# Optimization experiments

Measured on AMD Instinct MI355X. Metric: run time of the kernel, lower is better.

The kernel has to match this reference:

```python
import jax, jax.numpy as jnp
import numpy as np

N_EMBED = 1024
N_HEADS = 16
HEAD_DIM = N_EMBED // N_HEADS


def setup_inputs() -> dict:
    key = jax.random.key(0)
    ks = jax.random.split(key, 5)
    x = jax.random.normal(ks[0], (4, 2048, N_EMBED), dtype=jnp.float32)
    # Linear params (torch nn.Linear: y = x @ W.T + b); store W as [in, out]
    s = 1.0 / np.sqrt(N_EMBED)
    W_attn = jax.random.uniform(ks[1], (N_EMBED, 3 * N_EMBED), minval=-s, maxval=s, dtype=jnp.float32)
    b_attn = jax.random.uniform(ks[2], (3 * N_EMBED,), minval=-s, maxval=s, dtype=jnp.float32)
    W_proj = jax.random.uniform(ks[3], (N_EMBED, N_EMBED), minval=-s, maxval=s, dtype=jnp.float32)
    b_proj = jax.random.uniform(ks[4], (N_EMBED,), minval=-s, maxval=s, dtype=jnp.float32)
    return {"x": x, "W_attn": W_attn, "b_attn": b_attn, "W_proj": W_proj, "b_proj": b_proj}


def reference(x, W_attn, b_attn, W_proj, b_proj):
    B, L, D = x.shape
    H, Hd = N_HEADS, HEAD_DIM
    qkv = x @ W_attn + b_attn  # [B, L, 3D]
    q, k, v = jnp.split(qkv, 3, axis=-1)
    q = q.reshape(B, L, H, Hd).transpose(0, 2, 1, 3)  # [B, H, L, Hd]
    k = k.reshape(B, L, H, Hd).transpose(0, 2, 1, 3)
    v = v.reshape(B, L, H, Hd).transpose(0, 2, 1, 3)
    scores = jnp.einsum('bhqd,bhkd->bhqk', q, k) / jnp.sqrt(jnp.float32(Hd))
    causal = jnp.tril(jnp.ones((L, L), dtype=bool))
    scores = jnp.where(causal[None, None], scores, -jnp.inf)
    probs = jax.nn.softmax(scores.astype(jnp.float32), axis=-1).astype(x.dtype)
    o = jnp.einsum('bhqk,bhkd->bhqd', probs, v)  # [B, H, L, Hd]
    o = o.transpose(0, 2, 1, 3).reshape(B, L, D)
    return o @ W_proj + b_proj
```

## Files before the change

### kernel.cpp

```cpp
#include <hip/hip_runtime.h>


typedef __attribute__((ext_vector_type(8))) short short8;
typedef __attribute__((ext_vector_type(4))) short s16x4;
typedef __attribute__((ext_vector_type(4))) float f32x4;

#define DEVI __device__ __forceinline__

constexpr int NE = 1024, NH = 16, NB = 4, L = 2048;
constexpr int M = NB * L;
constexpr int KD = 1024;

DEVI unsigned f2bf(float f) {
    union { float f; unsigned u; } v; v.f = f;
    unsigned u = v.u;
    u += 0x7fffu + ((u >> 16) & 1u);
    return u >> 16;
}
DEVI unsigned pack_bf2(float lo, float hi) {
    union { float f; unsigned u; } a, b; a.f = lo; b.f = hi;
    return ((a.u + 0x8000u) >> 16) | ((b.u + 0x8000u) & 0xffff0000u);
}

typedef const __attribute__((address_space(1))) void* gas_t;
typedef __attribute__((address_space(3))) void* las_t;
DEVI void gl_lds16(const void* g, void* l) {
    __builtin_amdgcn_global_load_lds((gas_t)g, (las_t)l, 16, 0, 0);
}

__global__ void k_f32_to_bf16(const float* __restrict__ in,
                              unsigned short* __restrict__ out, int n8) {
    int i = blockIdx.x * blockDim.x + threadIdx.x;
    if (i >= n8) return;
    const float4* p = (const float4*)in + (size_t)i * 2;
    float4 a = p[0], b = p[1];
    short8 r;
    r[0] = f2bf(a.x); r[1] = f2bf(a.y); r[2] = f2bf(a.z); r[3] = f2bf(a.w);
    r[4] = f2bf(b.x); r[5] = f2bf(b.y); r[6] = f2bf(b.z); r[7] = f2bf(b.w);
    ((short8*)out)[i] = r;
}

__global__ void k_transpose_bf16(const float* __restrict__ in,
                                 unsigned short* __restrict__ out, int R, int C) {
    __shared__ float t[32][33];
    int x = blockIdx.x * 32 + threadIdx.x;
    int y0 = blockIdx.y * 32;
#pragma unroll
    for (int i = 0; i < 4; i++)
        t[threadIdx.y + 8 * i][threadIdx.x] = in[(size_t)(y0 + threadIdx.y + 8 * i) * C + x];
    __syncthreads();
    int xo = y0 + threadIdx.x;
    int yo = blockIdx.x * 32 + threadIdx.y;
#pragma unroll
    for (int i = 0; i < 4; i++)
        out[(size_t)(yo + 8 * i) * R + xo] = f2bf(t[threadIdx.x][threadIdx.y + 8 * i]);
}

template <int MODE>
__global__ __launch_bounds__(256, 4)
void k_gemm(const unsigned short* __restrict__ A,
            const unsigned short* __restrict__ Bt,
            const float* __restrict__ bias,
            unsigned short* __restrict__ Qb,
            unsigned short* __restrict__ Kb,
            unsigned short* __restrict__ Vt,
            float* __restrict__ out) {
    __shared__ alignas(16) short As[128 * 64];
    __shared__ alignas(16) short Bs[128 * 64];
    const int tid = threadIdx.x;
    const int lane = tid & 63, wid = tid >> 6;
    const int quad = lane >> 4, l16 = lane & 15;
    const int wm = (wid >> 1) * 64, wn = (wid & 1) * 64;
    const int m0 = blockIdx.y * 128;
    const int n0 = blockIdx.x * 128;

    const int srow = lane >> 3;
    const int gseg = (lane & 7) ^ srow;

    f32x4 acc[4][4] = {};

    for (int kk = 0; kk < KD; kk += 64) {
        __syncthreads();
#pragma unroll
        for (int c = 0; c < 4; c++) {
            const int rbase = c * 32 + wid * 8;
            gl_lds16(&A[(size_t)(m0 + rbase + srow) * KD + kk + gseg * 8], &As[rbase * 64]);
            gl_lds16(&Bt[(size_t)(n0 + rbase + srow) * KD + kk + gseg * 8], &Bs[rbase * 64]);
        }
        __syncthreads();
#pragma unroll
        for (int kc = 0; kc < 2; kc++) {
            short8 af[4], bf[4];
#pragma unroll
            for (int t = 0; t < 4; t++) {
                const int Ra = wm + t * 16 + l16;
                af[t] = *(const short8*)&As[Ra * 64 + (((kc * 4 + quad) ^ (Ra & 7)) * 8)];
                const int Rb = wn + t * 16 + l16;
                bf[t] = *(const short8*)&Bs[Rb * 64 + (((kc * 4 + quad) ^ (Rb & 7)) * 8)];
            }
#pragma unroll
            for (int mt = 0; mt < 4; mt++)
#pragma unroll
                for (int nt = 0; nt < 4; nt++)
                    acc[mt][nt] = __builtin_amdgcn_mfma_f32_16x16x32_bf16(
                        af[mt], bf[nt], acc[mt][nt], 0, 0, 0);
        }
    }

#pragma unroll
    for (int nt = 0; nt < 4; nt++) {
        const int n = n0 + wn + nt * 16 + l16;
        const float bv = bias[n];
        if (MODE == 0) {
            const int sel = n >> 10;
            const int h = (n & 1023) >> 6;
            const int d = n & 63;
#pragma unroll
            for (int mt = 0; mt < 4; mt++)
#pragma unroll
                for (int r = 0; r < 4; r++) {
                    const int m = m0 + wm + mt * 16 + quad * 4 + r;
                    const int b = m >> 11, l = m & 2047;
                    const int bh = b * NH + h;
                    const float v = acc[mt][nt][r] + bv;
                    if (sel == 0)      Qb[(size_t)(bh * L + l) * 64 + d] = f2bf(v * 0.125f);
                    else if (sel == 1) Kb[(size_t)(bh * L + l) * 64 + d] = f2bf(v);
                    else               Vt[(size_t)(bh * 64 + d) * L + l] = f2bf(v);
                }
        } else {
#pragma unroll
            for (int mt = 0; mt < 4; mt++)
#pragma unroll
                for (int r = 0; r < 4; r++) {
                    const int m = m0 + wm + mt * 16 + quad * 4 + r;
                    out[(size_t)m * NE + n] = acc[mt][nt][r] + bv;
                }
        }
    }
}

__global__ __launch_bounds__(256, 4)
void k_attn(const unsigned short* __restrict__ Q,
            const unsigned short* __restrict__ Kb,
            const unsigned short* __restrict__ Vt,
            unsigned short* __restrict__ O) {
    __shared__ alignas(16) short smem[16384];
    short* Ks = smem;
    short* Vs = smem + 8192;
    short* Os = smem;

    const int tid = threadIdx.x;
    const int lane = tid & 63, wid = tid >> 6;
    const int quad = lane >> 4, l16 = lane & 15;
    const int bh = blockIdx.x;
    const int qb = 15 - (int)blockIdx.y;
    const int q0 = qb * 128 + wid * 32;
    const size_t base = (size_t)bh * L * 64;
    const int b = bh >> 4, h = bh & 15;

    const int srowK = lane >> 3;
    const int gsegK = (lane & 7) ^ srowK;
    const int vrow_off = (lane >> 4);
    const int vseg = lane & 15;

    short8 qf[2][2];
#pragma unroll
    for (int mt = 0; mt < 2; mt++)
#pragma unroll
        for (int dc = 0; dc < 2; dc++)
            qf[mt][dc] = *(const short8*)&Q[base + (size_t)(q0 + mt * 16 + l16) * 64 + dc * 32 + quad * 8];

    f32x4 o[2][4] = {};
    float lrow[2] = {0.f, 0.f};

    for (int kt = 0; kt <= qb; kt++) {
        __syncthreads();
#pragma unroll
        for (int c = 0; c < 4; c++) {
            const int rbase = c * 32 + wid * 8;
            gl_lds16(&Kb[base + (size_t)(kt * 128 + rbase + srowK) * 64 + gsegK * 8],
                     &Ks[rbase * 64]);
        }
#pragma unroll
        for (int c = 0; c < 4; c++) {
            const int rbase = c * 16 + wid * 4;
            const int row = rbase + vrow_off;
            const int gs = vseg ^ (row & 15);
            gl_lds16(&Vt[base + (size_t)row * L + kt * 128 + gs * 8], &Vs[rbase * 128]);
        }
        __syncthreads();

        const bool diag = (kt == qb);
        const int chunks = diag ? (wid + 1) : 4;

        for (int kc = 0; kc < chunks; kc++) {
            short8 kf[2][2];
#pragma unroll
            for (int j0 = 0; j0 < 2; j0++)
#pragma unroll
                for (int dc = 0; dc < 2; dc++) {
                    const int R = kc * 32 + j0 * 16 + l16;
                    kf[j0][dc] = *(const short8*)&Ks[R * 64 + (((dc * 4 + quad) ^ (R & 7)) * 8)];
                }
            f32x4 st[2][2];
#pragma unroll
            for (int mt = 0; mt < 2; mt++)
#pragma unroll
                for (int j0 = 0; j0 < 2; j0++) {
                    f32x4 z = {};
                    z = __builtin_amdgcn_mfma_f32_16x16x32_bf16(kf[j0][0], qf[mt][0], z, 0, 0, 0);
                    z = __builtin_amdgcn_mfma_f32_16x16x32_bf16(kf[j0][1], qf[mt][1], z, 0, 0, 0);
                    st[mt][j0] = z;
                }
            const bool dm = diag && (kc == wid);
            short8 pb[2];
#pragma unroll
            for (int mt = 0; mt < 2; mt++) {
                float pe[8];
                float sum = 0.f;
#pragma unroll
                for (int j0 = 0; j0 < 2; j0++)
#pragma unroll
                    for (int r = 0; r < 4; r++) {
                        float p = __expf(st[mt][j0][r]);
                        if (dm) {
                            const int krel = j0 * 16 + quad * 4 + r;
                            const int qrel = mt * 16 + l16;
                            if (krel > qrel) p = 0.f;
                        }
                        sum += p;
                        pe[j0 * 4 + r] = p;
                    }
                lrow[mt] += sum;
#pragma unroll
                for (int w = 0; w < 4; w++) {
                    unsigned pk = pack_bf2(pe[2 * w], pe[2 * w + 1]);
                    pb[mt][2 * w] = (short)(pk & 0xffff);
                    pb[mt][2 * w + 1] = (short)(pk >> 16);
                }
            }
#pragma unroll
            for (int dt = 0; dt < 4; dt++) {
                const int R2 = dt * 16 + l16;
                const int s16a = kc * 4 + (quad >> 1);
                const int off = (quad & 1) * 4;
                s16x4 lo = *(const s16x4*)&Vs[R2 * 128 + ((s16a ^ l16) * 8) + off];
                s16x4 hi = *(const s16x4*)&Vs[R2 * 128 + (((s16a + 2) ^ l16) * 8) + off];
                short8 vf = __builtin_shufflevector(lo, hi, 0, 1, 2, 3, 4, 5, 6, 7);
#pragma unroll
                for (int mt = 0; mt < 2; mt++)
                    o[mt][dt] = __builtin_amdgcn_mfma_f32_16x16x32_bf16(
                        vf, pb[mt], o[mt][dt], 0, 0, 0);
            }
        }
    }

    float inv[2];
#pragma unroll
    for (int mt = 0; mt < 2; mt++) {
        float rs = lrow[mt];
        rs += __shfl_xor(rs, 16);
        rs += __shfl_xor(rs, 32);
        inv[mt] = 1.0f / rs;
    }

    __syncthreads();
#pragma unroll
    for (int mt = 0; mt < 2; mt++) {
        const int ql = wid * 32 + mt * 16 + l16;
#pragma unroll
        for (int dt = 0; dt < 4; dt++) {
            unsigned w0 = f2bf(o[mt][dt][0] * inv[mt]) | (f2bf(o[mt][dt][1] * inv[mt]) << 16);
            unsigned w1 = f2bf(o[mt][dt][2] * inv[mt]) | (f2bf(o[mt][dt][3] * inv[mt]) << 16);
            *(uint2*)&Os[ql * 72 + dt * 16 + quad * 4] = make_uint2(w0, w1);
        }
    }
    __syncthreads();
#pragma unroll
    for (int i = 0; i < 4; i++) {
        const int id = i * 256 + tid;
        const int row = id >> 3, seg = id & 7;
        short8 v = *(const short8*)&Os[row * 72 + seg * 8];
        const int q = qb * 128 + row;
        *(short8*)&O[(size_t)(b * L + q) * NE + h * 64 + seg * 8] = v;
    }
}

extern "C" void kernel_launch(void* const* d_in, const int* in_sizes, int n_in,
                              void* d_out, int out_size, void* d_ws, size_t ws_size,
                              hipStream_t stream) {
    const float* x  = (const float*)d_in[0];
    const float* Wa = (const float*)d_in[1];
    const float* ba = (const float*)d_in[2];
    const float* Wp = (const float*)d_in[3];
    const float* bp = (const float*)d_in[4];
    float* out = (float*)d_out;

    char* ws = (char*)d_ws;
    unsigned short* xb  = (unsigned short*)(ws);
    unsigned short* WaT = (unsigned short*)(ws + (16u << 20));
    unsigned short* WpT = (unsigned short*)(ws + (22u << 20));
    unsigned short* Qb  = (unsigned short*)(ws + (24u << 20));
    unsigned short* Kb  = (unsigned short*)(ws + (40u << 20));
    unsigned short* Vt  = (unsigned short*)(ws + (56u << 20));

    k_f32_to_bf16<<<(M * NE / 8 + 255) / 256, 256, 0, stream>>>(x, xb, M * NE / 8);
    k_transpose_bf16<<<dim3(3 * NE / 32, NE / 32), dim3(32, 8), 0, stream>>>(Wa, WaT, NE, 3 * NE);
    k_transpose_bf16<<<dim3(NE / 32, NE / 32), dim3(32, 8), 0, stream>>>(Wp, WpT, NE, NE);

    k_gemm<0><<<dim3(3 * NE / 128, M / 128), 256, 0, stream>>>(xb, WaT, ba, Qb, Kb, Vt, nullptr);

    unsigned short* Ob = xb;
    k_attn<<<dim3(NB * NH, 16), 256, 0, stream>>>(Qb, Kb, Vt, Ob);

    k_gemm<1><<<dim3(NE / 128, M / 128), 256, 0, stream>>>(Ob, WpT, bp, nullptr, nullptr, nullptr, out);
}
```

Measured before the change: 259.9 us.

## Double-buffer GEMM and attention LDS staging, enlarge attention query tile

The GEMM now splits each 64-wide K step into two 32-wide stages held in two LDS buffers. The next stage is fetched while MFMAs run on the current one. The attention kernel gives each block 256 queries (64 per wave) instead of 128 and double-buffers its K/V tiles so the next tile loads during compute. Causal masking now uses per-chunk absolute indices. The change targets global-load latency and doubles K/V reuse per load, at the cost of twice the LDS and registers in attention, which lowers occupancy (launch bounds go from 4 to 2).

```diff
diff --git a/kernel.cpp b/kernel.cpp
--- a/kernel.cpp
+++ b/kernel.cpp
@@ -65,8 +65,8 @@
             unsigned short* __restrict__ Kb,
             unsigned short* __restrict__ Vt,
             float* __restrict__ out) {
-    __shared__ alignas(16) short As[128 * 64];
-    __shared__ alignas(16) short Bs[128 * 64];
+    __shared__ alignas(16) short As[2][128 * 32];
+    __shared__ alignas(16) short Bs[2][128 * 32];
     const int tid = threadIdx.x;
     const int lane = tid & 63, wid = tid >> 6;
     const int quad = lane >> 4, l16 = lane & 15;
@@ -74,37 +74,46 @@
     const int m0 = blockIdx.y * 128;
     const int n0 = blockIdx.x * 128;
 
-    const int srow = lane >> 3;
-    const int gseg = (lane & 7) ^ srow;
+    const int srow = lane >> 2;
+    const int sseg = lane & 3;
 
     f32x4 acc[4][4] = {};
 
+    auto stage = [&](int buf, int kk) {
+#pragma unroll
+        for (int c = 0; c < 2; c++) {
+            const int rb = c * 64 + wid * 16;
+            const int row = rb + srow;
+            const int gs = sseg ^ (row & 3);
+            gl_lds16(&A[(size_t)(m0 + row) * KD + kk + gs * 8], &As[buf][rb * 32]);
+            gl_lds16(&Bt[(size_t)(n0 + row) * KD + kk + gs * 8], &Bs[buf][rb * 32]);
+        }
+    };
+    auto compute = [&](int buf) {
+        short8 af[4], bf[4];
+#pragma unroll
+        for (int t = 0; t < 4; t++) {
+            const int Ra = wm + t * 16 + l16;
+            af[t] = *(const short8*)&As[buf][Ra * 32 + ((quad ^ (Ra & 3)) * 8)];
+            const int Rb = wn + t * 16 + l16;
+            bf[t] = *(const short8*)&Bs[buf][Rb * 32 + ((quad ^ (Rb & 3)) * 8)];
+        }
+#pragma unroll
+        for (int mt = 0; mt < 4; mt++)
+#pragma unroll
+            for (int nt = 0; nt < 4; nt++)
+                acc[mt][nt] = __builtin_amdgcn_mfma_f32_16x16x32_bf16(
+                    af[mt], bf[nt], acc[mt][nt], 0, 0, 0);
+    };
+
+    stage(0, 0);
     for (int kk = 0; kk < KD; kk += 64) {
         __syncthreads();
-#pragma unroll
-        for (int c = 0; c < 4; c++) {
-            const int rbase = c * 32 + wid * 8;
-            gl_lds16(&A[(size_t)(m0 + rbase + srow) * KD + kk + gseg * 8], &As[rbase * 64]);
-            gl_lds16(&Bt[(size_t)(n0 + rbase + srow) * KD + kk + gseg * 8], &Bs[rbase * 64]);
-        }
+        if (kk + 32 < KD) stage(1, kk + 32);
+        compute(0);
         __syncthreads();
-#pragma unroll
-        for (int kc = 0; kc < 2; kc++) {
-            short8 af[4], bf[4];
-#pragma unroll
-            for (int t = 0; t < 4; t++) {
-                const int Ra = wm + t * 16 + l16;
-                af[t] = *(const short8*)&As[Ra * 64 + (((kc * 4 + quad) ^ (Ra & 7)) * 8)];
-                const int Rb = wn + t * 16 + l16;
-                bf[t] = *(const short8*)&Bs[Rb * 64 + (((kc * 4 + quad) ^ (Rb & 7)) * 8)];
-            }
-#pragma unroll
-            for (int mt = 0; mt < 4; mt++)
-#pragma unroll
-                for (int nt = 0; nt < 4; nt++)
-                    acc[mt][nt] = __builtin_amdgcn_mfma_f32_16x16x32_bf16(
-                        af[mt], bf[nt], acc[mt][nt], 0, 0, 0);
-        }
+        if (kk + 64 < KD) stage(0, kk + 64);
+        compute(1);
     }
 
 #pragma unroll
@@ -139,59 +148,65 @@
     }
 }
 
-__global__ __launch_bounds__(256, 4)
+__global__ __launch_bounds__(256, 2)
 void k_attn(const unsigned short* __restrict__ Q,
             const unsigned short* __restrict__ Kb,
             const unsigned short* __restrict__ Vt,
             unsigned short* __restrict__ O) {
-    __shared__ alignas(16) short smem[16384];
-    short* Ks = smem;
-    short* Vs = smem + 8192;
+    __shared__ alignas(16) short smem[32768];
+    short* Ksb = smem;
+    short* Vsb = smem + 16384;
     short* Os = smem;
 
     const int tid = threadIdx.x;
     const int lane = tid & 63, wid = tid >> 6;
     const int quad = lane >> 4, l16 = lane & 15;
     const int bh = blockIdx.x;
-    const int qb = 15 - (int)blockIdx.y;
-    const int q0 = qb * 128 + wid * 32;
+    const int qt = 7 - (int)blockIdx.y;
+    const int wq0 = qt * 256 + wid * 64;
     const size_t base = (size_t)bh * L * 64;
     const int b = bh >> 4, h = bh & 15;
 
-    const int srowK = lane >> 3;
-    const int gsegK = (lane & 7) ^ srowK;
-    const int vrow_off = (lane >> 4);
-    const int vseg = lane & 15;
-
-    short8 qf[2][2];
-#pragma unroll
-    for (int mt = 0; mt < 2; mt++)
+    short8 qf[4][2];
+#pragma unroll
+    for (int mt = 0; mt < 4; mt++)
 #pragma unroll
         for (int dc = 0; dc < 2; dc++)
-            qf[mt][dc] = *(const short8*)&Q[base + (size_t)(q0 + mt * 16 + l16) * 64 + dc * 32 + quad * 8];
-
-    f32x4 o[2][4] = {};
-    float lrow[2] = {0.f, 0.f};
-
-    for (int kt = 0; kt <= qb; kt++) {
+            qf[mt][dc] = *(const short8*)&Q[base + (size_t)(wq0 + mt * 16 + l16) * 64 + dc * 32 + quad * 8];
+
+    f32x4 o[4][4] = {};
+    float lrow[4] = {};
+
+    const int ntiles = 2 * qt + 2;
+
+    auto stage = [&](int buf, int kt) {
+        short* Kc = Ksb + buf * 8192;
+        short* Vc = Vsb + buf * 8192;
+#pragma unroll
+        for (int c = 0; c < 4; c++) {
+            const int rb = c * 32 + wid * 8;
+            const int row = rb + (lane >> 3);
+            const int gs = (lane & 7) ^ (row & 7);
+            gl_lds16(&Kb[base + (size_t)(kt * 128 + row) * 64 + gs * 8], &Kc[rb * 64]);
+        }
+#pragma unroll
+        for (int c = 0; c < 4; c++) {
+            const int rb = c * 16 + wid * 4;
+            const int row = rb + (lane >> 4);
+            const int gs = (lane & 15) ^ (row & 15);
+            gl_lds16(&Vt[base + (size_t)row * L + kt * 128 + gs * 8], &Vc[rb * 128]);
+        }
+    };
+
+    stage(0, 0);
+    for (int kt = 0; kt < ntiles; kt++) {
         __syncthreads();
-#pragma unroll
-        for (int c = 0; c < 4; c++) {
-            const int rbase = c * 32 + wid * 8;
-            gl_lds16(&Kb[base + (size_t)(kt * 128 + rbase + srowK) * 64 + gsegK * 8],
-                     &Ks[rbase * 64]);
-        }
-#pragma unroll
-        for (int c = 0; c < 4; c++) {
-            const int rbase = c * 16 + wid * 4;
-            const int row = rbase + vrow_off;
-            const int gs = vseg ^ (row & 15);
-            gl_lds16(&Vt[base + (size_t)row * L + kt * 128 + gs * 8], &Vs[rbase * 128]);
-        }
-        __syncthreads();
-
-        const bool diag = (kt == qb);
-        const int chunks = diag ? (wid + 1) : 4;
+        if (kt + 1 < ntiles) stage((kt + 1) & 1, kt + 1);
+        const short* Kc = Ksb + (kt & 1) * 8192;
+        const short* Vc = Vsb + (kt & 1) * 8192;
+
+        const int avail = wq0 + 64 - kt * 128;
+        const int chunks = avail <= 0 ? 0 : (avail >= 128 ? 4 : ((avail + 31) >> 5));
 
         for (int kc = 0; kc < chunks; kc++) {
             short8 kf[2][2];
@@ -200,11 +215,11 @@
 #pragma unroll
                 for (int dc = 0; dc < 2; dc++) {
                     const int R = kc * 32 + j0 * 16 + l16;
-                    kf[j0][dc] = *(const short8*)&Ks[R * 64 + (((dc * 4 + quad) ^ (R & 7)) * 8)];
-                }
-            f32x4 st[2][2];
-#pragma unroll
-            for (int mt = 0; mt < 2; mt++)
+                    kf[j0][dc] = *(const short8*)&Kc[R * 64 + (((dc * 4 + quad) ^ (R & 7)) * 8)];
+                }
+            f32x4 st[4][2];
+#pragma unroll
+            for (int mt = 0; mt < 4; mt++)
 #pragma unroll
                 for (int j0 = 0; j0 < 2; j0++) {
                     f32x4 z = {};
@@ -212,10 +227,10 @@
                     z = __builtin_amdgcn_mfma_f32_16x16x32_bf16(kf[j0][1], qf[mt][1], z, 0, 0, 0);
                     st[mt][j0] = z;
                 }
-            const bool dm = diag && (kc == wid);
-            short8 pb[2];
-#pragma unroll
-            for (int mt = 0; mt < 2; mt++) {
+            short8 pb[4];
+#pragma unroll
+            for (int mt = 0; mt < 4; mt++) {
+                const bool dm = (kt * 128 + kc * 32 + 31) > (wq0 + mt * 16);
                 float pe[8];
                 float sum = 0.f;
 #pragma unroll
@@ -224,9 +239,9 @@
                     for (int r = 0; r < 4; r++) {
                         float p = __expf(st[mt][j0][r]);
                         if (dm) {
-                            const int krel = j0 * 16 + quad * 4 + r;
-                            const int qrel = mt * 16 + l16;
-                            if (krel > qrel) p = 0.f;
+                            const int kcol = kt * 128 + kc * 32 + j0 * 16 + quad * 4 + r;
+                            const int q = wq0 + mt * 16 + l16;
+                            if (kcol > q) p = 0.f;
                         }
                         sum += p;
                         pe[j0 * 4 + r] = p;
@@ -244,20 +259,20 @@
                 const int R2 = dt * 16 + l16;
                 const int s16a = kc * 4 + (quad >> 1);
                 const int off = (quad & 1) * 4;
-                s16x4 lo = *(const s16x4*)&Vs[R2 * 128 + ((s16a ^ l16) * 8) + off];
-                s16x4 hi = *(const s16x4*)&Vs[R2 * 128 + (((s16a + 2) ^ l16) * 8) + off];
+                s16x4 lo = *(const s16x4*)&Vc[R2 * 128 + ((s16a ^ l16) * 8) + off];
+                s16x4 hi = *(const s16x4*)&Vc[R2 * 128 + (((s16a + 2) ^ l16) * 8) + off];
                 short8 vf = __builtin_shufflevector(lo, hi, 0, 1, 2, 3, 4, 5, 6, 7);
 #pragma unroll
-                for (int mt = 0; mt < 2; mt++)
+                for (int mt = 0; mt < 4; mt++)
                     o[mt][dt] = __builtin_amdgcn_mfma_f32_16x16x32_bf16(
                         vf, pb[mt], o[mt][dt], 0, 0, 0);
             }
         }
     }
 
-    float inv[2];
-#pragma unroll
-    for (int mt = 0; mt < 2; mt++) {
+    float inv[4];
+#pragma unroll
+    for (int mt = 0; mt < 4; mt++) {
         float rs = lrow[mt];
         rs += __shfl_xor(rs, 16);
         rs += __shfl_xor(rs, 32);
@@ -266,22 +281,22 @@
 
     __syncthreads();
 #pragma unroll
-    for (int mt = 0; mt < 2; mt++) {
-        const int ql = wid * 32 + mt * 16 + l16;
+    for (int mt = 0; mt < 4; mt++) {
+        const int lr = wid * 64 + mt * 16 + l16;
 #pragma unroll
         for (int dt = 0; dt < 4; dt++) {
             unsigned w0 = f2bf(o[mt][dt][0] * inv[mt]) | (f2bf(o[mt][dt][1] * inv[mt]) << 16);
             unsigned w1 = f2bf(o[mt][dt][2] * inv[mt]) | (f2bf(o[mt][dt][3] * inv[mt]) << 16);
-            *(uint2*)&Os[ql * 72 + dt * 16 + quad * 4] = make_uint2(w0, w1);
+            *(uint2*)&Os[lr * 72 + dt * 16 + quad * 4] = make_uint2(w0, w1);
         }
     }
     __syncthreads();
 #pragma unroll
-    for (int i = 0; i < 4; i++) {
+    for (int i = 0; i < 8; i++) {
         const int id = i * 256 + tid;
         const int row = id >> 3, seg = id & 7;
         short8 v = *(const short8*)&Os[row * 72 + seg * 8];
-        const int q = qb * 128 + row;
+        const int q = qt * 256 + row;
         *(short8*)&O[(size_t)(b * L + q) * NE + h * 64 + seg * 8] = v;
     }
 }
@@ -311,7 +326,7 @@
     k_gemm<0><<<dim3(3 * NE / 128, M / 128), 256, 0, stream>>>(xb, WaT, ba, Qb, Kb, Vt, nullptr);
 
     unsigned short* Ob = xb;
-    k_attn<<<dim3(NB * NH, 16), 256, 0, stream>>>(Qb, Kb, Vt, Ob);
+    k_attn<<<dim3(NB * NH, 8), 256, 0, stream>>>(Qb, Kb, Vt, Ob);
 
     k_gemm<1><<<dim3(NE / 128, M / 128), 256, 0, stream>>>(Ob, WpT, bp, nullptr, nullptr, nullptr, out);
 }
```

New measurement: 287.0 us. +10.4%, slower.
